# Optimization experiments

Measured on AMD Instinct MI355X. Metric: run time of the kernel, lower is better.

Reference implementation:

```python
import jax, jax.numpy as jnp
import numpy as np

D_MODEL = 2048
EXPAND = 2
INNER = EXPAND * D_MODEL          # 4096
HEADDIM = 64
NHEADS = INNER // HEADDIM         # 64
D_CONV = 4
BATCH, SEQLEN = 2, 4096


def setup_inputs() -> dict:
    key = jax.random.key(0)
    ks = jax.random.split(key, 12)
    f32 = jnp.float32
    return {
        "hidden_states": jax.random.normal(ks[0], (BATCH, SEQLEN, D_MODEL), f32),
        "in_proj_w": jax.random.normal(ks[1], (INNER, D_MODEL), f32) * 0.02,
        "gate_proj_w": jax.random.normal(ks[2], (INNER, D_MODEL), f32) * 0.02,
        "out_proj_w": jax.random.normal(ks[3], (D_MODEL, INNER), f32) * 0.02,
        "conv_weight": jax.random.normal(ks[4], (INNER, D_CONV), f32) * 0.02,
        "conv_bias": jnp.zeros((INNER,), f32),
        "dt_w": jax.random.normal(ks[5], (NHEADS, HEADDIM), f32) * 0.02,
        "dt_b": jnp.zeros((NHEADS,), f32),
        "A_log": jax.random.normal(ks[6], (NHEADS, HEADDIM), f32) * 0.1,
        "B": jax.random.normal(ks[7], (NHEADS, HEADDIM), f32) * 0.02,
        "C": jax.random.normal(ks[8], (NHEADS, HEADDIM), f32) * 0.02,
        "D": jnp.ones((NHEADS, HEADDIM), f32),
    }


def _dw_causal_conv_silu(x, w, b):
    # x: (B, L, C), w: (C, K), b: (C,). Causal depthwise conv + SiLU.
    K = w.shape[1]
    L = x.shape[1]
    xp = jnp.pad(x, ((0, 0), (K - 1, 0), (0, 0)))
    y = b
    for k in range(K):  # K=4, tiny fixed loop
        y = y + w[:, k] * xp[:, k:k + L, :]
    return jax.nn.silu(y)


def _diag_ssm_scan(a, u):
    # Linear recurrence s_t = a_t * s_{t-1} + u_t along axis=1 (seqlen).
    def comb(c1, c2):
        a1, b1 = c1
        a2, b2 = c2
        return a1 * a2, a2 * b1 + b2
    _, s = jax.lax.associative_scan(comb, (a, u), axis=1)
    return s


def reference(hidden_states, in_proj_w, gate_proj_w, out_proj_w,
              conv_weight, conv_bias, dt_w, dt_b, A_log, B, C, D):
    batch, seqlen, _ = hidden_states.shape
    projected = jnp.einsum('bld,cd->blc', hidden_states, in_proj_w)
    conv_out = _dw_causal_conv_silu(projected, conv_weight, conv_bias)
    gate = jax.nn.sigmoid(jnp.einsum('bld,cd->blc', hidden_states, gate_proj_w))

    X = conv_out.reshape(batch, seqlen, NHEADS, HEADDIM)
    dt = jax.nn.softplus(jnp.einsum('blhp,hp->blh', X, dt_w) + dt_b)  # (b,l,h)
    A = -jnp.exp(A_log)                                               # (h,p)

    a = jnp.exp(dt[..., None] * A)          # (b,l,h,p) decay factors
    u = dt[..., None] * B * X               # (b,l,h,p) driven input
    s = _diag_ssm_scan(a, u)                # (b,l,h,p) states
    y = C * s + D * X                       # (b,l,h,p)

    combined = y.reshape(batch, seqlen, INNER) * gate
    return jnp.einsum('blc,dc->bld', combined, out_proj_w)
```

## Files before the change

### kernel.cpp

```cpp
#include <hip/hip_runtime.h>
#include <cstdint>
#include <cstddef>

typedef unsigned short ushort;
typedef __attribute__((ext_vector_type(8))) short short8;
typedef __attribute__((ext_vector_type(8))) unsigned short ushort8;
typedef __attribute__((ext_vector_type(4))) float float4v;

#define DM    2048
#define INNERC 4096
#define LSEQ  4096
#define NBATCH 2
#define MROWS 8192
#define NHH   64
#define HDD   64
#define NCHUNK 32
#define CHLEN  128
#define CROWS 8

__device__ __forceinline__ float bf2f(ushort u) {
    return __uint_as_float(((unsigned int)u) << 16);
}
__device__ __forceinline__ ushort f2bf(float f) {
    unsigned int u = __float_as_uint(f);
    unsigned int r = u + 0x7FFFu + ((u >> 16) & 1u);
    return (ushort)(r >> 16);
}

__device__ __forceinline__ void async_cp16(const ushort* __restrict__ g, ushort* l) {
    __builtin_amdgcn_global_load_lds(
        (const __attribute__((address_space(1))) unsigned int*)g,
        (__attribute__((address_space(3))) unsigned int*)l,
        16, 0, 0);
}

__global__ void diag_kernel(float* __restrict__ out, float val) {
    if (threadIdx.x == 0 && blockIdx.x == 0) out[0] = val;
}

__global__ __launch_bounds__(256) void cast_bf16_kernel(
    const float* __restrict__ in, ushort* __restrict__ out, int n) {
    const int i = (blockIdx.x * 256 + threadIdx.x) * 8;
    if (i + 8 > n) return;
    const float4v a = *(const float4v*)(in + i);
    const float4v b = *(const float4v*)(in + i + 4);
    ushort8 o;
    o[0] = f2bf(a[0]); o[1] = f2bf(a[1]); o[2] = f2bf(a[2]); o[3] = f2bf(a[3]);
    o[4] = f2bf(b[0]); o[5] = f2bf(b[1]); o[6] = f2bf(b[2]); o[7] = f2bf(b[3]);
    *(ushort8*)(out + i) = o;
}


#define PH_PRE() do { \
    __builtin_amdgcn_s_barrier(); \
    asm volatile("s_waitcnt lgkmcnt(0)"); } while (0)

#define PH_POST() do { \
    __builtin_amdgcn_s_barrier(); } while (0)

#define MFMA_Q(AF, RBASE, CL) do { \
    __builtin_amdgcn_s_setprio(1); \
    _Pragma("unroll") for (int rm = 0; rm < 4; ++rm) \
    _Pragma("unroll") for (int cn = 0; cn < 2; ++cn) \
    _Pragma("unroll") for (int kk = 0; kk < 2; ++kk) \
        acc[(RBASE) + rm][(CL) + cn] = __builtin_amdgcn_mfma_f32_16x16x32_bf16( \
            AF[rm][kk], bf[(CL) + cn][kk], acc[(RBASE) + rm][(CL) + cn], 0, 0, 0); \
    __builtin_amdgcn_s_setprio(0); } while (0)

#define READ_A(DST, BUF, HB) do { \
    _Pragma("unroll") for (int rm = 0; rm < 4; ++rm) \
    _Pragma("unroll") for (int kk = 0; kk < 2; ++kk) { \
        const int rA = wm * 128 + (HB) * 64 + rm * 16 + l15; \
        DST[rm][kk] = *(const short8*)&As[BUF][ \
            (rA * 8 + ((kk * 4 + l4) ^ swz7)) * 8]; \
    } } while (0)

#define READ_B2(BUF, CNLO) do { \
    _Pragma("unroll") for (int cn = 0; cn < 2; ++cn) \
    _Pragma("unroll") for (int kk = 0; kk < 2; ++kk) { \
        const int rB = wn * 64 + ((CNLO) + cn) * 16 + l15; \
        bf[(CNLO) + cn][kk] = *(const short8*)&Bs[BUF][ \
            (rB * 8 + ((kk * 4 + l4) ^ swz7)) * 8]; \
    } } while (0)

template <int EPI>
__global__ __launch_bounds__(512, 2) void gemm256(
    const ushort* __restrict__ Ab, const ushort* __restrict__ Wb,
    void* __restrict__ Out, const ushort* __restrict__ Aux,
    int M, int N, int K) {
    __shared__ ushort As[2][16384];
    __shared__ ushort Bs[2][16384];

    const int tid  = threadIdx.x;
    const int lane = tid & 63;
    const int w    = tid >> 6;
    const int wm   = w >> 2;
    const int wn   = w & 3;
    const int l15  = lane & 15;
    const int l4   = lane >> 4;
    const int swz7 = l15 & 7;

    const int gx   = gridDim.x;
    const int nwg  = gx * gridDim.y;
    const int orig = blockIdx.y * gx + blockIdx.x;
    const int swz  = (orig & 7) * (nwg >> 3) + (orig >> 3);
    const int row0 = (swz / gx) * 256;
    const int col0 = (swz % gx) * 256;

    const int ni = K >> 7;

    float4v acc[8][4];
#pragma unroll
    for (int i2 = 0; i2 < 8; i2++)
#pragma unroll
        for (int j2 = 0; j2 < 4; j2++) {
            float4v z = {0.f, 0.f, 0.f, 0.f};
            acc[i2][j2] = z;
        }

    short8 afL[4][2], afH[4][2], bf[4][2];

    auto stage = [&](const ushort* __restrict__ G, int grow0, int t, ushort* dst) {
#pragma unroll
        for (int j = 0; j < 2; ++j) {
            const int c  = j * 512 + tid;
            const int r  = c >> 3;
            const int kg = (c & 7) ^ (r & 7);
            async_cp16(G + (size_t)(grow0 + r) * K + (t << 6) + kg * 8, dst + c * 8);
        }
    };

    stage(Ab, row0,       0, &As[0][0]);
    stage(Ab, row0 + 128, 0, &As[0][8192]);
    stage(Wb, col0,       0, &Bs[0][0]);
    stage(Wb, col0 + 128, 0, &Bs[0][8192]);
    stage(Ab, row0,       1, &As[1][0]);
    stage(Ab, row0 + 128, 1, &As[1][8192]);
    stage(Wb, col0,       1, &Bs[1][0]);
    stage(Wb, col0 + 128, 1, &Bs[1][8192]);
    asm volatile("s_waitcnt vmcnt(8)" ::: "memory");
    __builtin_amdgcn_s_barrier();

#pragma unroll 1
    for (int i = 0; i < ni; ++i) {
        const int u = 2 * i;
        const bool last = (i == ni - 1);

        READ_A(afL, 0, 0);
        READ_B2(0, 0);
        asm volatile("s_waitcnt lgkmcnt(8)");
        PH_PRE();
        MFMA_Q(afL, 0, 0);
        PH_POST();

        READ_B2(0, 2);
        PH_PRE();
        MFMA_Q(afL, 0, 2);
        PH_POST();

        READ_A(afH, 0, 1);
        if (!last) stage(Wb, col0, u + 2, &Bs[0][0]);
        PH_PRE();
        MFMA_Q(afH, 4, 2);
        PH_POST();

        if (!last) stage(Wb, col0 + 128, u + 2, &Bs[0][8192]);
        PH_PRE();
        MFMA_Q(afH, 4, 0);
        if (last) { asm volatile("s_waitcnt vmcnt(0)" ::: "memory"); }
        else      { asm volatile("s_waitcnt vmcnt(4)" ::: "memory"); }
        __builtin_amdgcn_s_barrier();

        READ_A(afL, 1, 0);
        READ_B2(1, 0);
        if (!last) stage(Ab, row0, u + 2, &As[0][0]);
        asm volatile("s_waitcnt lgkmcnt(8)");
        PH_PRE();
        MFMA_Q(afL, 0, 0);
        PH_POST();

        READ_B2(1, 2);
        if (!last) stage(Ab, row0 + 128, u + 2, &As[0][8192]);
        PH_PRE();
        MFMA_Q(afL, 0, 2);
        PH_POST();

        READ_A(afH, 1, 1);
        if (!last) {
            stage(Wb, col0,       u + 3, &Bs[1][0]);
            stage(Wb, col0 + 128, u + 3, &Bs[1][8192]);
        }
        PH_PRE();
        MFMA_Q(afH, 4, 2);
        PH_POST();

        if (!last) {
            stage(Ab, row0,       u + 3, &As[1][0]);
            stage(Ab, row0 + 128, u + 3, &As[1][8192]);
        }
        PH_PRE();
        MFMA_Q(afH, 4, 0);
        if (!last) { asm volatile("s_waitcnt vmcnt(8)" ::: "memory"); }
        __builtin_amdgcn_s_barrier();
    }

#pragma unroll
    for (int rm = 0; rm < 8; ++rm) {
#pragma unroll
        for (int cn = 0; cn < 4; ++cn) {
            const int r0 = row0 + wm * 128 + rm * 16 + l4 * 4;
            const int cc = col0 + wn * 64 + cn * 16 + l15;
#pragma unroll
            for (int rr = 0; rr < 4; ++rr) {
                const float v = acc[rm][cn][rr];
                const size_t off = (size_t)(r0 + rr) * N + cc;
                if (EPI == 0) {
                    ((ushort*)Out)[off] = f2bf(v);
                } else if (EPI == 1) {
                    const float g = 1.0f / (1.0f + __expf(-v));
                    ((ushort*)Out)[off] = f2bf(g * bf2f(Aux[off]));
                } else {
                    ((float*)Out)[off] = v;
                }
            }
        }
    }
}

__global__ __launch_bounds__(256) void conv_silu_kernel(
    const ushort* __restrict__ proj, const float* __restrict__ cw,
    const float* __restrict__ cb, ushort* __restrict__ X) {
    const int blk  = blockIdx.x;
    const int half = blk & 1;
    const int tile = blk >> 1;
    const int bl0  = tile * CROWS;
    const bool atStart = ((bl0 & (LSEQ - 1)) == 0);
    const int c0 = half * 2048 + threadIdx.x * 8;

    float4v w[8];
    const float4v* wp4 = (const float4v*)(cw + (size_t)c0 * 4);
#pragma unroll
    for (int t = 0; t < 8; t++) w[t] = wp4[t];
    float bias[8];
    const float4v b0 = *(const float4v*)(cb + c0);
    const float4v b1 = *(const float4v*)(cb + c0 + 4);
#pragma unroll
    for (int t = 0; t < 4; t++) { bias[t] = b0[t]; bias[t + 4] = b1[t]; }

    const size_t base = (size_t)bl0 * INNERC + c0;
    ushort8 w0, w1, w2;
    const ushort8 zz = {0, 0, 0, 0, 0, 0, 0, 0};
    if (atStart) {
        w0 = zz; w1 = zz; w2 = zz;
    } else {
        w0 = *(const ushort8*)(proj + base - 3 * (size_t)INNERC);
        w1 = *(const ushort8*)(proj + base - 2 * (size_t)INNERC);
        w2 = *(const ushort8*)(proj + base - 1 * (size_t)INNERC);
    }
#pragma unroll
    for (int r = 0; r < CROWS; r++) {
        const ushort8 cur = *(const ushort8*)(proj + base + (size_t)r * INNERC);
        ushort8 o;
#pragma unroll
        for (int j = 0; j < 8; j++) {
            const float acc = bias[j]
                + w[j][0] * bf2f(w0[j]) + w[j][1] * bf2f(w1[j])
                + w[j][2] * bf2f(w2[j]) + w[j][3] * bf2f(cur[j]);
            o[j] = f2bf(acc / (1.0f + __expf(-acc)));
        }
        *(ushort8*)(X + base + (size_t)r * INNERC) = o;
        w0 = w1; w1 = w2; w2 = cur;
    }
}

__global__ __launch_bounds__(64) void dt_kernel(
    const ushort* __restrict__ X, const float* __restrict__ dtw,
    const float* __restrict__ dtb, float* __restrict__ dt) {
    const int bl = blockIdx.x;
    const int h  = threadIdx.x;
    const ushort* xp = X + (size_t)bl * INNERC + h * 64;
    const float*  wp = dtw + h * 64;
    float acc = 0.0f;
#pragma unroll
    for (int p0 = 0; p0 < 64; p0 += 8) {
        const ushort8 xv = *(const ushort8*)(xp + p0);
#pragma unroll
        for (int j = 0; j < 8; j++) acc += bf2f(xv[j]) * wp[p0 + j];
    }
    const float z = acc + dtb[h];
    dt[bl * 64 + h] = (z > 20.0f) ? z : __logf(1.0f + __expf(z));
}

__global__ __launch_bounds__(256) void scan_pass1(
    const ushort* __restrict__ X, const float* __restrict__ dt,
    const float* __restrict__ A_log, const float* __restrict__ Bv,
    float* __restrict__ sumP, float* __restrict__ sumS) {
    const int task = blockIdx.x * 4 + (threadIdx.x >> 6);
    const int p  = threadIdx.x & 63;
    const int ch = task & (NCHUNK - 1);
    const int bh = task >> 5;
    const int h  = bh & 63;
    const int b  = bh >> 6;
    const float Ac = -__expf(A_log[h * 64 + p]);
    const float Bc = Bv[h * 64 + p];
    float Pr = 1.0f, s = 0.0f;
    const int bl0 = b * LSEQ + ch * CHLEN;
#pragma unroll 4
    for (int i = 0; i < CHLEN; i++) {
        const int bl   = bl0 + i;
        const float dtv = dt[bl * 64 + h];
        const float x   = bf2f(X[(size_t)bl * INNERC + h * 64 + p]);
        const float a   = __expf(dtv * Ac);
        Pr *= a;
        s = a * s + dtv * Bc * x;
    }
    sumP[(size_t)task * 64 + p] = Pr;
    sumS[(size_t)task * 64 + p] = s;
}

__global__ __launch_bounds__(64) void scan_pass2(
    const float* __restrict__ sumP, const float* __restrict__ sumS,
    float* __restrict__ carry) {
    const int bh = blockIdx.x;
    const int p  = threadIdx.x;
    float c = 0.0f;
    for (int ch = 0; ch < NCHUNK; ch++) {
        const size_t idx = ((size_t)bh * NCHUNK + ch) * 64 + p;
        carry[idx] = c;
        c = sumP[idx] * c + sumS[idx];
    }
}

__global__ __launch_bounds__(256) void scan_pass3(
    const ushort* __restrict__ X, const float* __restrict__ dt,
    const float* __restrict__ carry,
    const float* __restrict__ A_log, const float* __restrict__ Bv,
    const float* __restrict__ Cv, const float* __restrict__ Dv,
    ushort* __restrict__ Y) {
    const int task = blockIdx.x * 4 + (threadIdx.x >> 6);
    const int p  = threadIdx.x & 63;
    const int ch = task & (NCHUNK - 1);
    const int bh = task >> 5;
    const int h  = bh & 63;
    const int b  = bh >> 6;
    const float Ac = -__expf(A_log[h * 64 + p]);
    const float Bc = Bv[h * 64 + p];
    const float Cc = Cv[h * 64 + p];
    const float Dc = Dv[h * 64 + p];
    float s = carry[(size_t)task * 64 + p];
    const int bl0 = b * LSEQ + ch * CHLEN;
#pragma unroll 2
    for (int i = 0; i < CHLEN; i++) {
        const int bl = bl0 + i;
        const size_t xoff = (size_t)bl * INNERC + h * 64 + p;
        const float dtv = dt[bl * 64 + h];
        const float x   = bf2f(X[xoff]);
        const float a   = __expf(dtv * Ac);
        s = a * s + dtv * Bc * x;
        Y[xoff] = f2bf(Cc * s + Dc * x);
    }
}

#define OFF_PROJ  ((size_t)0)
#define OFF_HID   ((size_t)67108864)
#define OFF_WB    ((size_t)100663296)
#define OFF_DT    ((size_t)117440512)
#define OFF_SUMP  ((size_t)119537664)
#define OFF_SUMS  ((size_t)120586240)
#define OFF_CARRY ((size_t)121634816)
#define WS_NEEDED ((size_t)122683392)

extern "C" void kernel_launch(void* const* d_in, const int* in_sizes, int n_in,
                              void* d_out, int out_size, void* d_ws, size_t ws_size,
                              hipStream_t stream) {
    if (ws_size < WS_NEEDED) {
        diag_kernel<<<1, 64, 0, stream>>>((float*)d_out, (float)(ws_size >> 20));
        return;
    }
    const float* hidden = (const float*)d_in[0];
    const float* w_in   = (const float*)d_in[1];
    const float* w_gate = (const float*)d_in[2];
    const float* w_out  = (const float*)d_in[3];
    const float* conv_w = (const float*)d_in[4];
    const float* conv_b = (const float*)d_in[5];
    const float* dt_w   = (const float*)d_in[6];
    const float* dt_b   = (const float*)d_in[7];
    const float* A_log  = (const float*)d_in[8];
    const float* Bv     = (const float*)d_in[9];
    const float* Cv     = (const float*)d_in[10];
    const float* Dv     = (const float*)d_in[11];

    char* ws = (char*)d_ws;
    ushort* projbuf = (ushort*)(ws + OFF_PROJ);
    ushort* hid16   = (ushort*)(ws + OFF_HID);
    ushort* wbuf    = (ushort*)(ws + OFF_WB);
    float*  dtf     = (float*)(ws + OFF_DT);
    float*  sumP    = (float*)(ws + OFF_SUMP);
    float*  sumS    = (float*)(ws + OFF_SUMS);
    float*  carry   = (float*)(ws + OFF_CARRY);
    ushort* x16     = (ushort*)d_out;

    cast_bf16_kernel<<<8192, 256, 0, stream>>>(hidden, hid16, MROWS * DM);
    cast_bf16_kernel<<<4096, 256, 0, stream>>>(w_in, wbuf, INNERC * DM);

    gemm256<0><<<dim3(INNERC / 256, MROWS / 256), 512, 0, stream>>>(
        hid16, wbuf, projbuf, nullptr, MROWS, INNERC, DM);

    conv_silu_kernel<<<(MROWS / CROWS) * 2, 256, 0, stream>>>(projbuf, conv_w, conv_b, x16);
    dt_kernel<<<MROWS, 64, 0, stream>>>(x16, dt_w, dt_b, dtf);

    scan_pass1<<<(NBATCH * NHH * NCHUNK) / 4, 256, 0, stream>>>(
        x16, dtf, A_log, Bv, sumP, sumS);
    scan_pass2<<<NBATCH * NHH, 64, 0, stream>>>(sumP, sumS, carry);
    scan_pass3<<<(NBATCH * NHH * NCHUNK) / 4, 256, 0, stream>>>(
        x16, dtf, carry, A_log, Bv, Cv, Dv, projbuf);

    cast_bf16_kernel<<<4096, 256, 0, stream>>>(w_gate, wbuf, INNERC * DM);
    gemm256<1><<<dim3(INNERC / 256, MROWS / 256), 512, 0, stream>>>(
        hid16, wbuf, projbuf, projbuf, MROWS, INNERC, DM);

    cast_bf16_kernel<<<4096, 256, 0, stream>>>(w_out, wbuf, DM * INNERC);
    gemm256<2><<<dim3(DM / 256, MROWS / 256), 512, 0, stream>>>(
        projbuf, wbuf, d_out, nullptr, MROWS, DM, INNERC);
}
```

Baseline: 683.4 us.

## Fuse dt projection into conv kernel and streamline GEMM addressing and tail

Folds the dt projection and softplus into the conv+SiLU kernel using an 8-lane shuffle reduction, so the separate dt kernel and its re-read of X go away. The GEMM gets precomputed LDS read offsets, incremental 32-bit global offsets for async staging, a reordered MFMA loop with kk outermost, and a peeled last iteration that drops the per-iteration last-checks. Using 32-bit offsets assumes the matrix sizes stay under 4G elements. The peeled tail also drops the fine-grained phase barriers.

```diff
diff --git a/kernel.cpp b/kernel.cpp
--- a/kernel.cpp
+++ b/kernel.cpp
@@ -3,6 +3,7 @@
 #include <cstddef>
 
 typedef unsigned short ushort;
+typedef unsigned int uint;
 typedef __attribute__((ext_vector_type(8))) short short8;
 typedef __attribute__((ext_vector_type(8))) unsigned short ushort8;
 typedef __attribute__((ext_vector_type(4))) float float4v;
@@ -60,28 +61,29 @@
 
 #define MFMA_Q(AF, RBASE, CL) do { \
     __builtin_amdgcn_s_setprio(1); \
+    _Pragma("unroll") for (int kk = 0; kk < 2; ++kk) \
     _Pragma("unroll") for (int rm = 0; rm < 4; ++rm) \
     _Pragma("unroll") for (int cn = 0; cn < 2; ++cn) \
-    _Pragma("unroll") for (int kk = 0; kk < 2; ++kk) \
         acc[(RBASE) + rm][(CL) + cn] = __builtin_amdgcn_mfma_f32_16x16x32_bf16( \
             AF[rm][kk], bf[(CL) + cn][kk], acc[(RBASE) + rm][(CL) + cn], 0, 0, 0); \
     __builtin_amdgcn_s_setprio(0); } while (0)
 
 #define READ_A(DST, BUF, HB) do { \
-    _Pragma("unroll") for (int rm = 0; rm < 4; ++rm) \
-    _Pragma("unroll") for (int kk = 0; kk < 2; ++kk) { \
-        const int rA = wm * 128 + (HB) * 64 + rm * 16 + l15; \
-        DST[rm][kk] = *(const short8*)&As[BUF][ \
-            (rA * 8 + ((kk * 4 + l4) ^ swz7)) * 8]; \
+    _Pragma("unroll") for (int rm = 0; rm < 4; ++rm) { \
+        DST[rm][0] = *(const short8*)&As[BUF][offA_k0 + ((HB) * 4 + rm) * 1024]; \
+        DST[rm][1] = *(const short8*)&As[BUF][offA_k1 + ((HB) * 4 + rm) * 1024]; \
     } } while (0)
 
 #define READ_B2(BUF, CNLO) do { \
-    _Pragma("unroll") for (int cn = 0; cn < 2; ++cn) \
-    _Pragma("unroll") for (int kk = 0; kk < 2; ++kk) { \
-        const int rB = wn * 64 + ((CNLO) + cn) * 16 + l15; \
-        bf[(CNLO) + cn][kk] = *(const short8*)&Bs[BUF][ \
-            (rB * 8 + ((kk * 4 + l4) ^ swz7)) * 8]; \
+    _Pragma("unroll") for (int cn = 0; cn < 2; ++cn) { \
+        bf[(CNLO) + cn][0] = *(const short8*)&Bs[BUF][offB_k0 + ((CNLO) + cn) * 1024]; \
+        bf[(CNLO) + cn][1] = *(const short8*)&Bs[BUF][offB_k1 + ((CNLO) + cn) * 1024]; \
     } } while (0)
+
+#define STAGE(G, OFF, LBASE) do { \
+    async_cp16((G) + (OFF),       (LBASE) + (tid << 3)); \
+    async_cp16((G) + (OFF) + k64, (LBASE) + (tid << 3) + 4096); \
+    (OFF) += 64; } while (0)
 
 template <int EPI>
 __global__ __launch_bounds__(512, 2) void gemm256(
@@ -99,6 +101,8 @@
     const int l15  = lane & 15;
     const int l4   = lane >> 4;
     const int swz7 = l15 & 7;
+    const int s01  = swz7 & 3;
+    const int b2   = (swz7 >> 2) & 1;
 
     const int gx   = gridDim.x;
     const int nwg  = gx * gridDim.y;
@@ -109,6 +113,21 @@
 
     const int ni = K >> 7;
 
+    const int commA   = (wm * 128 + l15) * 64 + (l4 ^ s01) * 8;
+    const int offA_k0 = commA + (b2 ? 32 : 0);
+    const int offA_k1 = commA + (b2 ? 0 : 32);
+    const int commB   = (wn * 64 + l15) * 64 + (l4 ^ s01) * 8;
+    const int offB_k0 = commB + (b2 ? 32 : 0);
+    const int offB_k1 = commB + (b2 ? 0 : 32);
+
+    const uint rr8 = (uint)(tid >> 3);
+    const uint kg8 = (uint)(((tid & 7) ^ ((tid >> 3) & 7)) * 8);
+    const uint k64 = (uint)64 * (uint)K;
+    uint oA0 = (uint)(row0) * (uint)K + rr8 * (uint)K + kg8;
+    uint oA1 = oA0 + (uint)128 * (uint)K;
+    uint oW0 = (uint)(col0) * (uint)K + rr8 * (uint)K + kg8;
+    uint oW1 = oW0 + (uint)128 * (uint)K;
+
     float4v acc[8][4];
 #pragma unroll
     for (int i2 = 0; i2 < 8; i2++)
@@ -120,32 +139,19 @@
 
     short8 afL[4][2], afH[4][2], bf[4][2];
 
-    auto stage = [&](const ushort* __restrict__ G, int grow0, int t, ushort* dst) {
-#pragma unroll
-        for (int j = 0; j < 2; ++j) {
-            const int c  = j * 512 + tid;
-            const int r  = c >> 3;
-            const int kg = (c & 7) ^ (r & 7);
-            async_cp16(G + (size_t)(grow0 + r) * K + (t << 6) + kg * 8, dst + c * 8);
-        }
-    };
-
-    stage(Ab, row0,       0, &As[0][0]);
-    stage(Ab, row0 + 128, 0, &As[0][8192]);
-    stage(Wb, col0,       0, &Bs[0][0]);
-    stage(Wb, col0 + 128, 0, &Bs[0][8192]);
-    stage(Ab, row0,       1, &As[1][0]);
-    stage(Ab, row0 + 128, 1, &As[1][8192]);
-    stage(Wb, col0,       1, &Bs[1][0]);
-    stage(Wb, col0 + 128, 1, &Bs[1][8192]);
+    STAGE(Ab, oA0, &As[0][0]);
+    STAGE(Ab, oA1, &As[0][8192]);
+    STAGE(Wb, oW0, &Bs[0][0]);
+    STAGE(Wb, oW1, &Bs[0][8192]);
+    STAGE(Ab, oA0, &As[1][0]);
+    STAGE(Ab, oA1, &As[1][8192]);
+    STAGE(Wb, oW0, &Bs[1][0]);
+    STAGE(Wb, oW1, &Bs[1][8192]);
     asm volatile("s_waitcnt vmcnt(8)" ::: "memory");
     __builtin_amdgcn_s_barrier();
 
 #pragma unroll 1
-    for (int i = 0; i < ni; ++i) {
-        const int u = 2 * i;
-        const bool last = (i == ni - 1);
-
+    for (int i = 0; i < ni - 1; ++i) {
         READ_A(afL, 0, 0);
         READ_B2(0, 0);
         asm volatile("s_waitcnt lgkmcnt(8)");
@@ -159,49 +165,69 @@
         PH_POST();
 
         READ_A(afH, 0, 1);
-        if (!last) stage(Wb, col0, u + 2, &Bs[0][0]);
+        STAGE(Wb, oW0, &Bs[0][0]);
         PH_PRE();
         MFMA_Q(afH, 4, 2);
         PH_POST();
 
-        if (!last) stage(Wb, col0 + 128, u + 2, &Bs[0][8192]);
+        STAGE(Wb, oW1, &Bs[0][8192]);
         PH_PRE();
         MFMA_Q(afH, 4, 0);
-        if (last) { asm volatile("s_waitcnt vmcnt(0)" ::: "memory"); }
-        else      { asm volatile("s_waitcnt vmcnt(4)" ::: "memory"); }
+        asm volatile("s_waitcnt vmcnt(4)" ::: "memory");
         __builtin_amdgcn_s_barrier();
 
         READ_A(afL, 1, 0);
         READ_B2(1, 0);
-        if (!last) stage(Ab, row0, u + 2, &As[0][0]);
+        STAGE(Ab, oA0, &As[0][0]);
         asm volatile("s_waitcnt lgkmcnt(8)");
         PH_PRE();
         MFMA_Q(afL, 0, 0);
         PH_POST();
 
         READ_B2(1, 2);
-        if (!last) stage(Ab, row0 + 128, u + 2, &As[0][8192]);
+        STAGE(Ab, oA1, &As[0][8192]);
         PH_PRE();
         MFMA_Q(afL, 0, 2);
         PH_POST();
 
         READ_A(afH, 1, 1);
-        if (!last) {
-            stage(Wb, col0,       u + 3, &Bs[1][0]);
-            stage(Wb, col0 + 128, u + 3, &Bs[1][8192]);
-        }
+        STAGE(Wb, oW0, &Bs[1][0]);
+        STAGE(Wb, oW1, &Bs[1][8192]);
         PH_PRE();
         MFMA_Q(afH, 4, 2);
         PH_POST();
 
-        if (!last) {
-            stage(Ab, row0,       u + 3, &As[1][0]);
-            stage(Ab, row0 + 128, u + 3, &As[1][8192]);
-        }
+        STAGE(Ab, oA0, &As[1][0]);
+        STAGE(Ab, oA1, &As[1][8192]);
         PH_PRE();
         MFMA_Q(afH, 4, 0);
-        if (!last) { asm volatile("s_waitcnt vmcnt(8)" ::: "memory"); }
+        asm volatile("s_waitcnt vmcnt(8)" ::: "memory");
         __builtin_amdgcn_s_barrier();
+    }
+
+    {
+        READ_A(afL, 0, 0);
+        READ_B2(0, 0);
+        READ_B2(0, 2);
+        READ_A(afH, 0, 1);
+        __builtin_amdgcn_s_setprio(1);
+        MFMA_Q(afL, 0, 0);
+        MFMA_Q(afL, 0, 2);
+        MFMA_Q(afH, 4, 2);
+        MFMA_Q(afH, 4, 0);
+        __builtin_amdgcn_s_setprio(0);
+        asm volatile("s_waitcnt vmcnt(0)" ::: "memory");
+        __builtin_amdgcn_s_barrier();
+        READ_A(afL, 1, 0);
+        READ_B2(1, 0);
+        READ_B2(1, 2);
+        READ_A(afH, 1, 1);
+        __builtin_amdgcn_s_setprio(1);
+        MFMA_Q(afL, 0, 0);
+        MFMA_Q(afL, 0, 2);
+        MFMA_Q(afH, 4, 2);
+        MFMA_Q(afH, 4, 0);
+        __builtin_amdgcn_s_setprio(0);
     }
 
 #pragma unroll
@@ -229,13 +255,16 @@
 
 __global__ __launch_bounds__(256) void conv_silu_kernel(
     const ushort* __restrict__ proj, const float* __restrict__ cw,
-    const float* __restrict__ cb, ushort* __restrict__ X) {
+    const float* __restrict__ cb, const float* __restrict__ dtw,
+    const float* __restrict__ dtb, ushort* __restrict__ X,
+    float* __restrict__ dt) {
     const int blk  = blockIdx.x;
     const int half = blk & 1;
     const int tile = blk >> 1;
     const int bl0  = tile * CROWS;
     const bool atStart = ((bl0 & (LSEQ - 1)) == 0);
     const int c0 = half * 2048 + threadIdx.x * 8;
+    const int h  = c0 >> 6;
 
     float4v w[8];
     const float4v* wp4 = (const float4v*)(cw + (size_t)c0 * 4);
@@ -246,6 +275,13 @@
     const float4v b1 = *(const float4v*)(cb + c0 + 4);
 #pragma unroll
     for (int t = 0; t < 4; t++) { bias[t] = b0[t]; bias[t + 4] = b1[t]; }
+
+    float dtwv[8];
+    const float4v d0 = *(const float4v*)(dtw + c0);
+    const float4v d1 = *(const float4v*)(dtw + c0 + 4);
+#pragma unroll
+    for (int t = 0; t < 4; t++) { dtwv[t] = d0[t]; dtwv[t + 4] = d1[t]; }
+    const float dtbv = dtb[h];
 
     const size_t base = (size_t)bl0 * INNERC + c0;
     ushort8 w0, w1, w2;
@@ -261,34 +297,26 @@
     for (int r = 0; r < CROWS; r++) {
         const ushort8 cur = *(const ushort8*)(proj + base + (size_t)r * INNERC);
         ushort8 o;
+        float dacc = 0.0f;
 #pragma unroll
         for (int j = 0; j < 8; j++) {
             const float acc = bias[j]
                 + w[j][0] * bf2f(w0[j]) + w[j][1] * bf2f(w1[j])
                 + w[j][2] * bf2f(w2[j]) + w[j][3] * bf2f(cur[j]);
-            o[j] = f2bf(acc / (1.0f + __expf(-acc)));
+            const float s = acc / (1.0f + __expf(-acc));
+            o[j] = f2bf(s);
+            dacc += s * dtwv[j];
         }
         *(ushort8*)(X + base + (size_t)r * INNERC) = o;
+        dacc += __shfl_xor(dacc, 1, 64);
+        dacc += __shfl_xor(dacc, 2, 64);
+        dacc += __shfl_xor(dacc, 4, 64);
+        if ((threadIdx.x & 7) == 0) {
+            const float z = dacc + dtbv;
+            dt[(bl0 + r) * 64 + h] = (z > 20.0f) ? z : __logf(1.0f + __expf(z));
+        }
         w0 = w1; w1 = w2; w2 = cur;
     }
-}
-
-__global__ __launch_bounds__(64) void dt_kernel(
-    const ushort* __restrict__ X, const float* __restrict__ dtw,
-    const float* __restrict__ dtb, float* __restrict__ dt) {
-    const int bl = blockIdx.x;
-    const int h  = threadIdx.x;
-    const ushort* xp = X + (size_t)bl * INNERC + h * 64;
-    const float*  wp = dtw + h * 64;
-    float acc = 0.0f;
-#pragma unroll
-    for (int p0 = 0; p0 < 64; p0 += 8) {
-        const ushort8 xv = *(const ushort8*)(xp + p0);
-#pragma unroll
-        for (int j = 0; j < 8; j++) acc += bf2f(xv[j]) * wp[p0 + j];
-    }
-    const float z = acc + dtb[h];
-    dt[bl * 64 + h] = (z > 20.0f) ? z : __logf(1.0f + __expf(z));
 }
 
 __global__ __launch_bounds__(256) void scan_pass1(
@@ -406,8 +434,8 @@
     gemm256<0><<<dim3(INNERC / 256, MROWS / 256), 512, 0, stream>>>(
         hid16, wbuf, projbuf, nullptr, MROWS, INNERC, DM);
 
-    conv_silu_kernel<<<(MROWS / CROWS) * 2, 256, 0, stream>>>(projbuf, conv_w, conv_b, x16);
-    dt_kernel<<<MROWS, 64, 0, stream>>>(x16, dt_w, dt_b, dtf);
+    conv_silu_kernel<<<(MROWS / CROWS) * 2, 256, 0, stream>>>(
+        projbuf, conv_w, conv_b, dt_w, dt_b, x16, dtf);
 
     scan_pass1<<<(NBATCH * NHH * NCHUNK) / 4, 256, 0, stream>>>(
         x16, dtf, A_log, Bv, sumP, sumS);
```

New measurement: 647.5 us. 1.06x faster.
